# Optimization experiments

Hardware: AMD Instinct MI355X
Metric: run time of the kernel (lower is better)

The kernel has to match this reference:

```python
import jax, jax.numpy as jnp
import numpy as np


def setup_inputs() -> dict:
    key = jax.random.key(0)
    k1, k2, k3 = jax.random.split(key, 3)
    p = 4096
    target = jax.random.normal(k1, (p, p), dtype=jnp.float32)
    source = jax.random.normal(k2, (p, p), dtype=jnp.float32)
    W_beta = jax.random.uniform(k3, (p, p), dtype=jnp.float32)
    return {"target": target, "source": source, "W_beta": W_beta}


def reference(target, source, W_beta):
    # X = target, Y = source (module-level names in the original).
    # denominator inner loop: sum_i X[i] . X[i] == ||X||_F^2 (scalar),
    # recomputed p^2 times in the original; computed once here.
    s = jnp.sum(target * target)
    W = W_beta.sum(axis=1)                       # [p]
    W2 = W * W                                   # [p]
    scale = W2 / (s * W2 + 1.0)                  # [p]
    G = jnp.matmul(source, target.T)             # [p,p], G[i,j] = Y[i] . X[j]
    W_matrix = scale[:, None] * G                # [p,p]
    primary = jnp.matmul(W_matrix, target) - source
    loss = jnp.sqrt(jnp.sum(jnp.square(jnp.matmul(W_beta, primary))))
    return loss, W_matrix
```

## Files before the change

### kernel.cpp

```cpp
#include <hip/hip_runtime.h>
#include <hip/hip_bf16.h>

#define PDIM 4096
#define PPN ((size_t)PDIM * (size_t)PDIM)

typedef __attribute__((ext_vector_type(8))) short bf16x8;
typedef __attribute__((ext_vector_type(4))) float floatx4;
typedef __attribute__((ext_vector_type(8))) int int8v;

__device__ __forceinline__ void load_lds16(const void* g, void* l) {
  __builtin_amdgcn_global_load_lds(
      (const __attribute__((address_space(1))) void*)g,
      (__attribute__((address_space(3))) void*)l, 16, 0, 0);
}

__device__ __forceinline__ unsigned short bf16bits(float f) {
  __hip_bfloat16 h = __float2bfloat16(f);
  return *(unsigned short*)&h;
}

__device__ __forceinline__ unsigned char fp8byte(float v) {
  return (unsigned char)(__builtin_amdgcn_cvt_pk_fp8_f32(v, v, 0, false) & 0xff);
}
__device__ __forceinline__ unsigned int fp8x4(float a, float b, float c, float d) {
  int v = __builtin_amdgcn_cvt_pk_fp8_f32(a, b, 0, false);
  v = __builtin_amdgcn_cvt_pk_fp8_f32(c, d, v, true);
  return (unsigned int)v;
}

__global__ void sumsq(const float4* __restrict__ x, float* __restrict__ acc) {
  float s = 0.f;
  const size_t n4 = PPN / 4;
  for (size_t i = (size_t)blockIdx.x * 256 + threadIdx.x; i < n4;
       i += (size_t)gridDim.x * 256) {
    const float4 v = x[i];
    s += v.x * v.x + v.y * v.y + v.z * v.z + v.w * v.w;
  }
#pragma unroll
  for (int off = 32; off > 0; off >>= 1) s += __shfl_down(s, off);
  __shared__ float ws[4];
  if ((threadIdx.x & 63) == 0) ws[threadIdx.x >> 6] = s;
  __syncthreads();
  if (threadIdx.x == 0) atomicAdd(acc, ws[0] + ws[1] + ws[2] + ws[3]);
}

__global__ void cast_x(const float* __restrict__ src,
                       __hip_bfloat16* __restrict__ dstN,
                       unsigned char* __restrict__ dstT8) {
  __shared__ float tile[64][65];
  const int bx = blockIdx.x * 64, by = blockIdx.y * 64;
  const int tx = threadIdx.x & 15, ty = threadIdx.x >> 4;
#pragma unroll
  for (int r = 0; r < 4; ++r) {
    const int row = ty + r * 16;
    const float4 v = *(const float4*)&src[(size_t)(by + row) * PDIM + bx + tx * 4];
    tile[row][tx * 4 + 0] = v.x;
    tile[row][tx * 4 + 1] = v.y;
    tile[row][tx * 4 + 2] = v.z;
    tile[row][tx * 4 + 3] = v.w;
    ushort4 o;
    o.x = bf16bits(v.x); o.y = bf16bits(v.y); o.z = bf16bits(v.z); o.w = bf16bits(v.w);
    *(ushort4*)&dstN[(size_t)(by + row) * PDIM + bx + tx * 4] = o;
  }
  __syncthreads();
#pragma unroll
  for (int r = 0; r < 4; ++r) {
    const int i = ty + r * 16;
    *(unsigned int*)&dstT8[(size_t)(bx + i) * PDIM + by + tx * 4] =
        fp8x4(tile[tx * 4 + 0][i], tile[tx * 4 + 1][i],
              tile[tx * 4 + 2][i], tile[tx * 4 + 3][i]);
  }
}

__global__ void cast_y(const float* __restrict__ src,
                       __hip_bfloat16* __restrict__ dstN,
                       __hip_bfloat16* __restrict__ dstT) {
  __shared__ float tile[64][65];
  const int bx = blockIdx.x * 64, by = blockIdx.y * 64;
  const int tx = threadIdx.x & 15, ty = threadIdx.x >> 4;
#pragma unroll
  for (int r = 0; r < 4; ++r) {
    const int row = ty + r * 16;
    const float4 v = *(const float4*)&src[(size_t)(by + row) * PDIM + bx + tx * 4];
    tile[row][tx * 4 + 0] = v.x;
    tile[row][tx * 4 + 1] = v.y;
    tile[row][tx * 4 + 2] = v.z;
    tile[row][tx * 4 + 3] = v.w;
    ushort4 o;
    o.x = bf16bits(v.x); o.y = bf16bits(v.y); o.z = bf16bits(v.z); o.w = bf16bits(v.w);
    *(ushort4*)&dstN[(size_t)(by + row) * PDIM + bx + tx * 4] = o;
  }
  __syncthreads();
#pragma unroll
  for (int r = 0; r < 4; ++r) {
    const int i = ty + r * 16;
    ushort4 o;
    o.x = bf16bits(tile[tx * 4 + 0][i]);
    o.y = bf16bits(tile[tx * 4 + 1][i]);
    o.z = bf16bits(tile[tx * 4 + 2][i]);
    o.w = bf16bits(tile[tx * 4 + 3][i]);
    *(ushort4*)&dstT[(size_t)(bx + i) * PDIM + by + tx * 4] = o;
  }
}

__global__ void cast_wb_rows(const float* __restrict__ Wb,
                             unsigned char* __restrict__ Wb8,
                             const float* __restrict__ sAcc,
                             float* __restrict__ scale) {
  const size_t row = blockIdx.x;
  const float4* src = (const float4*)(Wb + row * PDIM);
  unsigned int* dst = (unsigned int*)(Wb8 + row * PDIM);
  float sum = 0.f;
#pragma unroll
  for (int it = 0; it < 4; ++it) {
    const int j = threadIdx.x + it * 256;
    const float4 v = src[j];
    sum += (v.x + v.y) + (v.z + v.w);
    dst[j] = fp8x4(v.x, v.y, v.z, v.w);
  }
#pragma unroll
  for (int off = 32; off > 0; off >>= 1) sum += __shfl_down(sum, off);
  __shared__ float ws[4];
  if ((threadIdx.x & 63) == 0) ws[threadIdx.x >> 6] = sum;
  __syncthreads();
  if (threadIdx.x == 0) {
    const float W = ws[0] + ws[1] + ws[2] + ws[3];
    const float w2 = W * W;
    scale[row] = w2 / ((*sAcc) * w2 + 1.0f);
  }
}

__device__ __forceinline__ void mfma_quad(floatx4 (&acc)[8][4], int mo, int no,
                                          const bf16x8 (&af)[8],
                                          const bf16x8 (&bf)[4]) {
  __builtin_amdgcn_s_setprio(1);
#pragma unroll
  for (int mi = 0; mi < 4; ++mi)
#pragma unroll
    for (int ni = 0; ni < 2; ++ni)
#pragma unroll
      for (int kk = 0; kk < 2; ++kk)
        acc[mo + mi][no + ni] = __builtin_amdgcn_mfma_f32_16x16x32_bf16(
            af[mi * 2 + kk], bf[ni * 2 + kk], acc[mo + mi][no + ni], 0, 0, 0);
  __builtin_amdgcn_s_setprio(0);
}

__global__ __launch_bounds__(512, 2)
void gemm_bf16_wm(const __hip_bfloat16* __restrict__ A,
                  const __hip_bfloat16* __restrict__ B,
                  const float* __restrict__ scale,
                  float* __restrict__ outF,
                  unsigned char* __restrict__ Wm8) {
  __shared__ __align__(16) char LDS[131072];

  const int tid = threadIdx.x;
  const int lane = tid & 63;
  const int wave = tid >> 6;
  const int wm = wave >> 2;
  const int wn = wave & 3;

  const int bid = blockIdx.x;
  const int swz = (bid & 7) * 32 + (bid >> 3);
  const int bx = swz & 15;
  const int by = swz >> 4;
  const size_t rowA0 = (size_t)by * 256;
  const size_t rowB0 = (size_t)bx * 256;

  const int srow = tid >> 3;
  const int scol = ((tid & 7) ^ (srow & 7)) << 4;
  const char* pA = (const char*)A + (rowA0 + srow) * 8192 + scol;
  const char* pB = (const char*)B + (rowB0 + srow) * 8192 + scol;
  const int ldsWav = wave * 1024;

  const int fr = lane & 15;
  const int kq = lane >> 4;
  const int slot0 = ((kq ^ (fr & 7)) << 4);
  const int aRowB = (wm * 64 + fr) * 128;
  const int bRowB = (wn * 32 + fr) * 128;

  floatx4 acc[8][4] = {};
  bf16x8 af[8], bLo[4], bHi[4];

  {
    char* dA0 = LDS + ldsWav;
    char* dB0 = LDS + 65536 + ldsWav;
    load_lds16(pA, dA0);
    load_lds16(pA + 524288, dA0 + 8192);
    load_lds16(pB, dB0);
    load_lds16(pB + 524288, dB0 + 8192);
    load_lds16(pB + 1048576, dB0 + 16384);
    load_lds16(pB + 1048576 + 524288, dB0 + 16384 + 8192);
    load_lds16(pA + 1048576, dA0 + 16384);
    load_lds16(pA + 1048576 + 524288, dA0 + 16384 + 8192);
    char* dA1 = dA0 + 32768;
    char* dB1 = dB0 + 32768;
    load_lds16(pA + 128, dA1);
    load_lds16(pA + 128 + 524288, dA1 + 8192);
    load_lds16(pB + 128, dB1);
    load_lds16(pB + 128 + 524288, dB1 + 8192);
    load_lds16(pB + 128 + 1048576, dB1 + 16384);
    load_lds16(pB + 128 + 1048576 + 524288, dB1 + 16384 + 8192);
    load_lds16(pA + 128 + 1048576, dA1 + 16384);
    load_lds16(pA + 128 + 1048576 + 524288, dA1 + 16384 + 8192);
  }
  asm volatile("s_waitcnt vmcnt(8)" ::: "memory");
  __builtin_amdgcn_s_barrier();

  for (int t = 0; t < 64; ++t) {
    const int buf = (t & 1) << 15;
    const int tS = (t + 2) & 63;
    const char* sA = pA + (size_t)tS * 128;
    const char* sB = pB + (size_t)tS * 128;
    char* dA = LDS + buf + ldsWav;
    char* dB = LDS + 65536 + buf + ldsWav;
    const char* aRd = LDS + buf + aRowB;
    const char* bRd = LDS + 65536 + buf + bRowB;

#pragma unroll
    for (int mi = 0; mi < 4; ++mi) {
      af[mi * 2 + 0] = *(const bf16x8*)(aRd + mi * 2048 + slot0);
      af[mi * 2 + 1] = *(const bf16x8*)(aRd + mi * 2048 + (slot0 ^ 64));
    }
#pragma unroll
    for (int ni = 0; ni < 2; ++ni) {
      bLo[ni * 2 + 0] = *(const bf16x8*)(bRd + ni * 2048 + slot0);
      bLo[ni * 2 + 1] = *(const bf16x8*)(bRd + ni * 2048 + (slot0 ^ 64));
    }
    load_lds16(sA, dA);
    load_lds16(sA + 524288, dA + 8192);
    asm volatile("s_waitcnt lgkmcnt(8)" ::: "memory");
    __builtin_amdgcn_s_barrier();
    asm volatile("s_waitcnt lgkmcnt(0)" ::: "memory");
    __builtin_amdgcn_sched_barrier(0);
    mfma_quad(acc, 0, 0, af, bLo);
    __builtin_amdgcn_s_barrier();

#pragma unroll
    for (int ni = 0; ni < 2; ++ni) {
      bHi[ni * 2 + 0] = *(const bf16x8*)(bRd + 16384 + ni * 2048 + slot0);
      bHi[ni * 2 + 1] = *(const bf16x8*)(bRd + 16384 + ni * 2048 + (slot0 ^ 64));
    }
    load_lds16(sB, dB);
    load_lds16(sB + 524288, dB + 8192);
    __builtin_amdgcn_s_barrier();
    asm volatile("s_waitcnt lgkmcnt(0)" ::: "memory");
    __builtin_amdgcn_sched_barrier(0);
    mfma_quad(acc, 0, 2, af, bHi);
    __builtin_amdgcn_s_barrier();

#pragma unroll
    for (int mi = 0; mi < 4; ++mi) {
      af[mi * 2 + 0] = *(const bf16x8*)(aRd + 16384 + mi * 2048 + slot0);
      af[mi * 2 + 1] = *(const bf16x8*)(aRd + 16384 + mi * 2048 + (slot0 ^ 64));
    }
    load_lds16(sB + 1048576, dB + 16384);
    load_lds16(sB + 1048576 + 524288, dB + 16384 + 8192);
    __builtin_amdgcn_s_barrier();
    asm volatile("s_waitcnt lgkmcnt(0)" ::: "memory");
    __builtin_amdgcn_sched_barrier(0);
    mfma_quad(acc, 4, 2, af, bHi);
    __builtin_amdgcn_s_barrier();

    asm volatile("s_waitcnt vmcnt(6)" ::: "memory");
    __builtin_amdgcn_sched_barrier(0);
    load_lds16(sA + 1048576, dA + 16384);
    load_lds16(sA + 1048576 + 524288, dA + 16384 + 8192);
    __builtin_amdgcn_s_barrier();
    mfma_quad(acc, 4, 0, af, bLo);
    __builtin_amdgcn_s_barrier();
  }

  const int lr = (lane >> 4) << 2;
  const int lc = lane & 15;
#pragma unroll
  for (int mi = 0; mi < 8; ++mi) {
    const size_t rbase = rowA0 + (size_t)(mi >> 2) * 128 + wm * 64 + (mi & 3) * 16 + lr;
#pragma unroll
    for (int r = 0; r < 4; ++r) {
      const size_t row = rbase + r;
      const float sc = scale[row];
#pragma unroll
      for (int ni = 0; ni < 4; ++ni) {
        const size_t col = rowB0 + (size_t)(ni >> 1) * 128 + wn * 32 + (ni & 1) * 16 + lc;
        const float v = sc * acc[mi][ni][r];
        outF[row * PDIM + col] = v;
        Wm8[row * PDIM + col] = fp8byte(v * 131072.f);
      }
    }
  }
}

template <int MODE>
__global__ __launch_bounds__(256)
void gemm_fp8(const unsigned char* __restrict__ A,
              const unsigned char* __restrict__ B,
              const __hip_bfloat16* __restrict__ sub,
              unsigned char* __restrict__ outP,
              float* __restrict__ lossAcc) {
  __shared__ __align__(16) unsigned char As[128 * 128];
  __shared__ __align__(16) unsigned char Bs[128 * 128];

  const int tid = threadIdx.x;
  const int lane = tid & 63;
  const int wave = tid >> 6;
  const int wm = wave >> 1, wn = wave & 1;

  const size_t rowA0 = (size_t)blockIdx.y * 128;
  const size_t rowB0 = (size_t)blockIdx.x * 128;

  const unsigned char* gA[4];
  const unsigned char* gB[4];
  int ldsOff[4];
#pragma unroll
  for (int m = 0; m < 4; ++m) {
    const int ci = tid + m * 256;
    const int r = ci >> 3, s = ci & 7;
    const int cg = s ^ (r & 7);
    gA[m] = A + (rowA0 + (size_t)r) * PDIM + cg * 16;
    gB[m] = B + (rowB0 + (size_t)r) * PDIM + cg * 16;
    ldsOff[m] = m * 4096 + wave * 1024;
  }

  floatx4 acc[4][4] = {};

  const int fr = lane & 15;
  const int e = fr & 7;
  const int q2 = (lane >> 4) << 1;
  const int offLo = (q2 ^ e) << 4;
  const int offHi = ((q2 + 1) ^ e) << 4;
  const int abase = (wm * 64 + fr) * 128;
  const int bbase = (wn * 64 + fr) * 128;

  for (int kt = 0; kt < PDIM; kt += 128) {
#pragma unroll
    for (int m = 0; m < 4; ++m) load_lds16(gA[m] + kt, (char*)As + ldsOff[m]);
#pragma unroll
    for (int m = 0; m < 4; ++m) load_lds16(gB[m] + kt, (char*)Bs + ldsOff[m]);
    __syncthreads();

    union { int8v v; int4 h[2]; } af[4], bg[4];
#pragma unroll
    for (int mi = 0; mi < 4; ++mi) {
      af[mi].h[0] = *(const int4*)(As + abase + mi * 2048 + offLo);
      af[mi].h[1] = *(const int4*)(As + abase + mi * 2048 + offHi);
    }
#pragma unroll
    for (int ni = 0; ni < 4; ++ni) {
      bg[ni].h[0] = *(const int4*)(Bs + bbase + ni * 2048 + offLo);
      bg[ni].h[1] = *(const int4*)(Bs + bbase + ni * 2048 + offHi);
    }
#pragma unroll
    for (int mi = 0; mi < 4; ++mi)
#pragma unroll
      for (int ni = 0; ni < 4; ++ni)
        acc[mi][ni] = __builtin_amdgcn_mfma_scale_f32_16x16x128_f8f6f4(
            af[mi].v, bg[ni].v, acc[mi][ni],
            0 , 0 , 0, 0x7F7F7F7F, 0, 0x7F7F7F7F);
    __syncthreads();
  }

  const size_t row0 = rowA0 + wm * 64;
  const size_t col0 = rowB0 + wn * 64;
  const int lr = (lane >> 4) << 2;
  const int lc = lane & 15;

  if constexpr (MODE == 2) {
    float tot = 0.f;
#pragma unroll
    for (int mi = 0; mi < 4; ++mi)
#pragma unroll
      for (int ni = 0; ni < 4; ++ni)
#pragma unroll
        for (int r = 0; r < 4; ++r) tot += acc[mi][ni][r] * acc[mi][ni][r];
#pragma unroll
    for (int off = 32; off > 0; off >>= 1) tot += __shfl_down(tot, off);
    __shared__ float ws[4];
    if (lane == 0) ws[wave] = tot;
    __syncthreads();
    if (tid == 0) atomicAdd(lossAcc, ws[0] + ws[1] + ws[2] + ws[3]);
  } else {
    constexpr float INV = 1.f / 131072.f;
#pragma unroll
    for (int mi = 0; mi < 4; ++mi) {
#pragma unroll
      for (int r = 0; r < 4; ++r) {
        const size_t row = row0 + mi * 16 + lr + r;
#pragma unroll
        for (int ni = 0; ni < 4; ++ni) {
          const size_t col = col0 + ni * 16 + lc;
          const float v = acc[mi][ni][r] * INV - __bfloat162float(sub[row * PDIM + col]);
          outP[row * PDIM + col] = fp8byte(v);
        }
      }
    }
  }
}

__global__ void finalize(float* __restrict__ out, const float* __restrict__ acc) {
  if (threadIdx.x == 0) out[0] = sqrtf(*acc);
}

extern "C" void kernel_launch(void* const* d_in, const int* in_sizes, int n_in,
                              void* d_out, int out_size, void* d_ws, size_t ws_size,
                              hipStream_t stream) {
  const float* X  = (const float*)d_in[0];
  const float* Y  = (const float*)d_in[1];
  const float* Wb = (const float*)d_in[2];
  float* out = (float*)d_out;

  __hip_bfloat16* Xb   = (__hip_bfloat16*)d_ws;
  __hip_bfloat16* Yb   = Xb + PPN;
  __hip_bfloat16* YbT  = Yb + PPN;
  unsigned char*  XT8  = (unsigned char*)(YbT + PPN);
  unsigned char*  Wm8  = XT8 + PPN;
  unsigned char*  Wb8  = Wm8 + PPN;
  unsigned char*  PT8  = Wb8 + PPN;
  float* scale   = (float*)(PT8 + PPN);
  float* sAcc    = scale + PDIM;
  float* lossAcc = sAcc + 1;

  hipMemsetAsync(sAcc, 0, 2 * sizeof(float), stream);

  sumsq<<<1024, 256, 0, stream>>>((const float4*)X, sAcc);

  dim3 cgrid(PDIM / 64, PDIM / 64);
  cast_x<<<cgrid, 256, 0, stream>>>(X, Xb, XT8);
  cast_y<<<cgrid, 256, 0, stream>>>(Y, Yb, YbT);
  cast_wb_rows<<<PDIM, 256, 0, stream>>>(Wb, Wb8, sAcc, scale);

  gemm_bf16_wm<<<dim3(256), 512, 0, stream>>>(Yb, Xb, scale, out + 1, Wm8);

  dim3 ggrid(PDIM / 128, PDIM / 128);
  gemm_fp8<1><<<ggrid, 256, 0, stream>>>(XT8, Wm8, YbT, PT8, nullptr);
  gemm_fp8<2><<<ggrid, 256, 0, stream>>>(PT8, Wb8, nullptr, nullptr, lossAcc);

  finalize<<<1, 1, 0, stream>>>(out, lossAcc);
}
```

Baseline: 541.0 us.

## Software-pipeline LDS fragment reads against MFMA with register double buffering

The bf16 GEMM main loop now keeps separate Lo/Hi A-fragment registers and issues the LDS reads for the next quadrant (including the first fragments of the next k-tile from the other LDS buffer) right after each MFMA quad. Before, each phase waited on lgkmcnt and a sched_barrier before its MFMAs. A prologue preloads the first fragments. The aim is to hide LDS read latency behind MFMA work and cut stalls between phases. In exchange it uses more VGPRs, which could hurt occupancy at 2 blocks per CU, and the changed vmcnt waits must still order correctly against the global-to-LDS loads.

```diff
diff --git a/kernel.cpp b/kernel.cpp
--- a/kernel.cpp
+++ b/kernel.cpp
@@ -145,6 +145,21 @@
   __builtin_amdgcn_s_setprio(0);
 }
 
+__device__ __forceinline__ void read_a(bf16x8 (&dst)[8], const char* base, int slot0) {
+#pragma unroll
+  for (int mi = 0; mi < 4; ++mi) {
+    dst[mi * 2 + 0] = *(const bf16x8*)(base + mi * 2048 + slot0);
+    dst[mi * 2 + 1] = *(const bf16x8*)(base + mi * 2048 + (slot0 ^ 64));
+  }
+}
+__device__ __forceinline__ void read_b(bf16x8 (&dst)[4], const char* base, int slot0) {
+#pragma unroll
+  for (int ni = 0; ni < 2; ++ni) {
+    dst[ni * 2 + 0] = *(const bf16x8*)(base + ni * 2048 + slot0);
+    dst[ni * 2 + 1] = *(const bf16x8*)(base + ni * 2048 + (slot0 ^ 64));
+  }
+}
+
 __global__ __launch_bounds__(512, 2)
 void gemm_bf16_wm(const __hip_bfloat16* __restrict__ A,
                   const __hip_bfloat16* __restrict__ B,
@@ -179,31 +194,27 @@
   const int bRowB = (wn * 32 + fr) * 128;
 
   floatx4 acc[8][4] = {};
-  bf16x8 af[8], bLo[4], bHi[4];
+  bf16x8 afLo[8], afHi[8], bLo[4], bHi[4];
 
   {
     char* dA0 = LDS + ldsWav;
     char* dB0 = LDS + 65536 + ldsWav;
-    load_lds16(pA, dA0);
-    load_lds16(pA + 524288, dA0 + 8192);
-    load_lds16(pB, dB0);
-    load_lds16(pB + 524288, dB0 + 8192);
-    load_lds16(pB + 1048576, dB0 + 16384);
-    load_lds16(pB + 1048576 + 524288, dB0 + 16384 + 8192);
-    load_lds16(pA + 1048576, dA0 + 16384);
-    load_lds16(pA + 1048576 + 524288, dA0 + 16384 + 8192);
+    load_lds16(pA, dA0);                         load_lds16(pA + 524288, dA0 + 8192);
+    load_lds16(pB, dB0);                         load_lds16(pB + 524288, dB0 + 8192);
+    load_lds16(pB + 1048576, dB0 + 16384);       load_lds16(pB + 1572864, dB0 + 24576);
+    load_lds16(pA + 1048576, dA0 + 16384);       load_lds16(pA + 1572864, dA0 + 24576);
     char* dA1 = dA0 + 32768;
     char* dB1 = dB0 + 32768;
-    load_lds16(pA + 128, dA1);
-    load_lds16(pA + 128 + 524288, dA1 + 8192);
-    load_lds16(pB + 128, dB1);
-    load_lds16(pB + 128 + 524288, dB1 + 8192);
-    load_lds16(pB + 128 + 1048576, dB1 + 16384);
-    load_lds16(pB + 128 + 1048576 + 524288, dB1 + 16384 + 8192);
-    load_lds16(pA + 128 + 1048576, dA1 + 16384);
-    load_lds16(pA + 128 + 1048576 + 524288, dA1 + 16384 + 8192);
+    load_lds16(pA + 128, dA1);                   load_lds16(pA + 128 + 524288, dA1 + 8192);
+    load_lds16(pB + 128, dB1);                   load_lds16(pB + 128 + 524288, dB1 + 8192);
+    load_lds16(pB + 128 + 1048576, dB1 + 16384); load_lds16(pB + 128 + 1572864, dB1 + 24576);
+    load_lds16(pA + 128 + 1048576, dA1 + 16384); load_lds16(pA + 128 + 1572864, dA1 + 24576);
   }
   asm volatile("s_waitcnt vmcnt(8)" ::: "memory");
+  __builtin_amdgcn_s_barrier();
+  read_a(afLo, (const char*)LDS + aRowB, slot0);
+  read_b(bLo, (const char*)LDS + 65536 + bRowB, slot0);
+  asm volatile("s_waitcnt lgkmcnt(0)" ::: "memory");
   __builtin_amdgcn_s_barrier();
 
   for (int t = 0; t < 64; ++t) {
@@ -213,60 +224,35 @@
     const char* sB = pB + (size_t)tS * 128;
     char* dA = LDS + buf + ldsWav;
     char* dB = LDS + 65536 + buf + ldsWav;
-    const char* aRd = LDS + buf + aRowB;
-    const char* bRd = LDS + 65536 + buf + bRowB;
-
-#pragma unroll
-    for (int mi = 0; mi < 4; ++mi) {
-      af[mi * 2 + 0] = *(const bf16x8*)(aRd + mi * 2048 + slot0);
-      af[mi * 2 + 1] = *(const bf16x8*)(aRd + mi * 2048 + (slot0 ^ 64));
-    }
-#pragma unroll
-    for (int ni = 0; ni < 2; ++ni) {
-      bLo[ni * 2 + 0] = *(const bf16x8*)(bRd + ni * 2048 + slot0);
-      bLo[ni * 2 + 1] = *(const bf16x8*)(bRd + ni * 2048 + (slot0 ^ 64));
-    }
+    const char* aRd  = LDS + buf + aRowB;
+    const char* bRd  = LDS + 65536 + buf + bRowB;
+    const char* aRdN = LDS + (buf ^ 32768) + aRowB;
+    const char* bRdN = LDS + 65536 + (buf ^ 32768) + bRowB;
+
     load_lds16(sA, dA);
     load_lds16(sA + 524288, dA + 8192);
-    asm volatile("s_waitcnt lgkmcnt(8)" ::: "memory");
+    mfma_quad(acc, 0, 0, afLo, bLo);
+    read_b(bHi, bRd + 16384, slot0);
     __builtin_amdgcn_s_barrier();
-    asm volatile("s_waitcnt lgkmcnt(0)" ::: "memory");
-    __builtin_amdgcn_sched_barrier(0);
-    mfma_quad(acc, 0, 0, af, bLo);
-    __builtin_amdgcn_s_barrier();
-
-#pragma unroll
-    for (int ni = 0; ni < 2; ++ni) {
-      bHi[ni * 2 + 0] = *(const bf16x8*)(bRd + 16384 + ni * 2048 + slot0);
-      bHi[ni * 2 + 1] = *(const bf16x8*)(bRd + 16384 + ni * 2048 + (slot0 ^ 64));
-    }
+
     load_lds16(sB, dB);
     load_lds16(sB + 524288, dB + 8192);
+    mfma_quad(acc, 0, 2, afLo, bHi);
+    read_a(afHi, aRd + 16384, slot0);
     __builtin_amdgcn_s_barrier();
-    asm volatile("s_waitcnt lgkmcnt(0)" ::: "memory");
-    __builtin_amdgcn_sched_barrier(0);
-    mfma_quad(acc, 0, 2, af, bHi);
+
+    asm volatile("s_waitcnt vmcnt(10)" ::: "memory");
+    load_lds16(sB + 1048576, dB + 16384);
+    load_lds16(sB + 1572864, dB + 24576);
+    mfma_quad(acc, 4, 2, afHi, bHi);
+    read_a(afLo, aRdN, slot0);
     __builtin_amdgcn_s_barrier();
 
-#pragma unroll
-    for (int mi = 0; mi < 4; ++mi) {
-      af[mi * 2 + 0] = *(const bf16x8*)(aRd + 16384 + mi * 2048 + slot0);
-      af[mi * 2 + 1] = *(const bf16x8*)(aRd + 16384 + mi * 2048 + (slot0 ^ 64));
-    }
-    load_lds16(sB + 1048576, dB + 16384);
-    load_lds16(sB + 1048576 + 524288, dB + 16384 + 8192);
-    __builtin_amdgcn_s_barrier();
-    asm volatile("s_waitcnt lgkmcnt(0)" ::: "memory");
-    __builtin_amdgcn_sched_barrier(0);
-    mfma_quad(acc, 4, 2, af, bHi);
-    __builtin_amdgcn_s_barrier();
-
     asm volatile("s_waitcnt vmcnt(6)" ::: "memory");
-    __builtin_amdgcn_sched_barrier(0);
     load_lds16(sA + 1048576, dA + 16384);
-    load_lds16(sA + 1048576 + 524288, dA + 16384 + 8192);
-    __builtin_amdgcn_s_barrier();
-    mfma_quad(acc, 4, 0, af, bLo);
+    load_lds16(sA + 1572864, dA + 24576);
+    mfma_quad(acc, 4, 0, afHi, bLo);
+    read_b(bLo, bRdN, slot0);
     __builtin_amdgcn_s_barrier();
   }
 
```

New measurement: 541.1 us. No clear change (+0.0%).
